# Optimization experiments

Measured on AMD Instinct MI355X. Metric: run time of the kernel, lower is better.

## Reference

```python
import jax, jax.numpy as jnp
import numpy as np

VOCAB, EMBED, SEQ, HID = 50000, 128, 200, 30
BATCH = 4096


def setup_inputs() -> dict:
    key = jax.random.key(0)
    ks = jax.random.split(key, 14)
    s = lambda fan_in: 1.0 / np.sqrt(fan_in)
    return {
        "tokens": jax.random.randint(ks[0], (BATCH, SEQ), 0, VOCAB, dtype=jnp.int32),
        "emb": jax.random.normal(ks[1], (VOCAB, EMBED), jnp.float32) * 0.05,
        "Wx": jax.random.normal(ks[2], (EMBED, HID), jnp.float32) * s(EMBED),
        "Wh": jax.random.normal(ks[3], (HID, HID), jnp.float32) * s(HID),
        "b_rnn": jnp.zeros((HID,), jnp.float32),
        "W1": jax.random.normal(ks[4], (HID, 128), jnp.float32) * s(HID),
        "b1": jnp.zeros((128,), jnp.float32),
        "W2": jax.random.normal(ks[5], (128, 64), jnp.float32) * s(128),
        "b2": jnp.zeros((64,), jnp.float32),
        "W3": jax.random.normal(ks[6], (64, 32), jnp.float32) * s(64),
        "b3": jnp.zeros((32,), jnp.float32),
        "Wo": jax.random.normal(ks[7], (32, 1), jnp.float32) * s(32),
        "bo": jnp.zeros((1,), jnp.float32),
    }


def reference(tokens, emb, Wx, Wh, b_rnn, W1, b1, W2, b2, W3, b3, Wo, bo):
    # Embedding lookup: [B, T, E]
    x = emb[tokens]
    # SimpleRNN (tanh), return last hidden state. Precompute input projection
    # once as a big GEMM, then scan the recurrence over time.
    xp = jnp.einsum("bte,eh->tbh", x, Wx) + b_rnn  # [T, B, H]
    h0 = jnp.zeros((tokens.shape[0], Wh.shape[0]), x.dtype)

    def step(h, xp_t):
        h_new = jnp.tanh(xp_t + h @ Wh)
        return h_new, None

    h_last, _ = jax.lax.scan(step, h0, xp)
    # Dense head (dropout layers are identity at inference).
    d1 = jax.nn.relu(h_last @ W1 + b1)
    d2 = jax.nn.relu(d1 @ W2 + b2)
    d3 = jax.nn.relu(d2 @ W3 + b3)
    return jax.nn.sigmoid(d3 @ Wo + bo)
```

## Files before the change

### kernel.cpp

```cpp
#include <hip/hip_runtime.h>
#include <math.h>

#define VOCAB 50000
#define EMBED 128
#define SEQ   200
#define HID   30
#define BATCH 4096

typedef float4 __attribute__((__may_alias__)) f4ma;
typedef unsigned int uint2v __attribute__((ext_vector_type(2)));

__device__ __forceinline__ float tanh_fast(float x) {
    float e = __expf(2.0f * x);
    return 1.0f - __fdividef(2.0f, e + 1.0f);
}
__device__ __forceinline__ float swz16_f(float x) {
    return __int_as_float(__builtin_amdgcn_ds_swizzle(__float_as_int(x), 0x401F));
}

__global__ __launch_bounds__(256, 2) void embproj_kernel(
    const float* __restrict__ emb, const float* __restrict__ Wx,
    const float* __restrict__ brnn, float* __restrict__ embP)
{
    int tid  = threadIdx.x;
    int wv   = tid >> 6;
    int l    = tid & 63;
    int j16  = l & 15;
    int p    = (l >> 4) & 1;
    int g    = l >> 5;
    int col  = j16 + 16 * g;
    int colc = (col < HID) ? col : (HID - 1);
    int k0   = 64 * p;

    float whx[64];
    #pragma unroll
    for (int i = 0; i < 64; ++i)
        whx[i] = Wx[(k0 + i) * HID + colc];
    float bj = brnn[colc];

    int base = (blockIdx.x * 4 + wv) * 25;

    float4 eA[16], eB[16];
    #define LOADROW(dst, v) { \
        int vc = min((v), VOCAB - 1); \
        const f4ma* e4 = (const f4ma*)(emb + (size_t)vc * EMBED + k0); \
        _Pragma("unroll") \
        for (int q = 0; q < 16; ++q) dst[q] = e4[q]; \
    }
    #define COMPUTE(src, v) { \
        float a0 = 0.f, a1 = 0.f, a2 = 0.f, a3 = 0.f; \
        _Pragma("unroll") \
        for (int q = 0; q < 16; ++q) { \
            a0 += src[q].x * whx[4*q+0]; \
            a1 += src[q].y * whx[4*q+1]; \
            a2 += src[q].z * whx[4*q+2]; \
            a3 += src[q].w * whx[4*q+3]; \
        } \
        float own  = (a0 + a1) + (a2 + a3); \
        float full = bj + (own + swz16_f(own)); \
        if (p == 0 && col < HID && (v) < VOCAB) \
            embP[(size_t)(v) * HID + col] = full; \
    }

    LOADROW(eA, base + 0);
    for (int r = 0; r < 25; r += 2) {
        LOADROW(eB, base + r + 1);
        COMPUTE(eA, base + r);
        LOADROW(eA, base + r + 2);
        COMPUTE(eB, base + r + 1);
    }
    #undef LOADROW
    #undef COMPUTE
}

__global__ __launch_bounds__(128) void rnn_head_kernel(
    const int* __restrict__ tokens, const float* __restrict__ embP,
    const float* __restrict__ Wh,
    const float* __restrict__ W1, const float* __restrict__ b1,
    const float* __restrict__ W2, const float* __restrict__ b2,
    const float* __restrict__ W3, const float* __restrict__ b3,
    const float* __restrict__ Wo, const float* __restrict__ bo,
    float* __restrict__ out)
{
    __shared__ __align__(16) float hL[4][32];
    __shared__ float d1L[4][128];
    __shared__ float d2L[4][64];

    int tid  = threadIdx.x;
    int wv   = tid >> 6;
    int l    = tid & 63;
    int j16  = l & 15;
    int row  = (l >> 4) & 1;
    int p    = l >> 5;
    int j    = j16 + 16 * p;
    int rloc = wv * 2 + row;
    int b    = blockIdx.x * 4 + rloc;

    const int* trow = tokens + (size_t)b * SEQ;
    int jc = (j < HID) ? j : (HID - 1);

    hL[rloc][j] = 0.0f;
    __builtin_amdgcn_sched_barrier(0);

    bool useR0;
    {
        unsigned li = (unsigned)l;
        uint2v rp = __builtin_amdgcn_permlane32_swap(li, li, false, false);
        useR0 = (rp[0] == (unsigned)(l ^ 32));
    }

    int cB = j16 + 16;
    float whA[16], whB[16];
    #pragma unroll
    for (int kk = 0; kk < 16; ++kk) {
        int k = 16 * p + kk;
        whA[kk] = (k < HID) ? Wh[k * HID + j16] : 0.0f;
        whB[kk] = (k < HID && cB < HID) ? Wh[k * HID + cB] : 0.0f;
    }

    float xq[8]; int tr[8];
    #pragma unroll
    for (int s = 0; s < 8; ++s) {
        xq[s] = embP[(size_t)trow[s] * HID + jc];
        tr[s] = trow[8 + s];
    }

    for (int t = 0; t < SEQ; t += 8) {
        #pragma unroll
        for (int s = 0; s < 8; ++s) {
            float hv[16];
            const f4ma* h4 = (const f4ma*)(&hL[rloc][16 * p]);
            #pragma unroll
            for (int qq = 0; qq < 4; ++qq) {
                f4ma hh = h4[qq];
                hv[4*qq+0] = hh.x; hv[4*qq+1] = hh.y;
                hv[4*qq+2] = hh.z; hv[4*qq+3] = hh.w;
            }
            float xp = xq[s];
            xq[s] = embP[(size_t)tr[s] * HID + jc];
            int tn = t + 16 + s; tn = (tn < SEQ) ? tn : SEQ - 1;
            tr[s] = trow[tn];

            float a0=0.f, a1=0.f, b0=0.f, b1=0.f;
            #pragma unroll
            for (int kk = 0; kk < 16; kk += 2) {
                a0 += hv[kk]   * whA[kk];
                a1 += hv[kk+1] * whA[kk+1];
                b0 += hv[kk]   * whB[kk];
                b1 += hv[kk+1] * whB[kk+1];
            }
            float pA = a0 + a1;
            float pB = b0 + b1;
            float own  = p ? pB : pA;
            float send = p ? pA : pB;
            unsigned si = __float_as_uint(send);
            uint2v sw = __builtin_amdgcn_permlane32_swap(si, si, false, false);
            float recv = __uint_as_float(useR0 ? sw[0] : sw[1]);
            float hn = tanh_fast(xp + (own + recv));
            if (j < HID) hL[rloc][j] = hn;
            __builtin_amdgcn_sched_barrier(0);
        }
    }

    {
        int half = l >> 5, j32 = l & 31;
        int rh = wv * 2 + half;
        int bB = blockIdx.x * 4 + rh;
        #pragma unroll
        for (int qq = 0; qq < 4; ++qq) {
            int c = j32 + 32 * qq;
            float acc = b1[c];
            #pragma unroll
            for (int k = 0; k < HID; ++k) acc += hL[rh][k] * W1[k * 128 + c];
            d1L[rh][c] = fmaxf(acc, 0.0f);
        }
        #pragma unroll
        for (int qq = 0; qq < 2; ++qq) {
            int c = j32 + 32 * qq;
            float acc = b2[c];
            #pragma unroll 8
            for (int k = 0; k < 128; ++k) acc += d1L[rh][k] * W2[k * 64 + c];
            d2L[rh][c] = fmaxf(acc, 0.0f);
        }
        float acc3 = b3[j32];
        #pragma unroll 8
        for (int k = 0; k < 64; ++k) acc3 += d2L[rh][k] * W3[k * 32 + j32];
        acc3 = fmaxf(acc3, 0.0f);
        float prod = acc3 * Wo[j32];
        #pragma unroll
        for (int m = 16; m > 0; m >>= 1) prod += __shfl_xor(prod, m, 32);
        if (j32 == 0) out[bB] = 1.0f / (1.0f + __expf(-(prod + bo[0])));
    }
}

extern "C" void kernel_launch(void* const* d_in, const int* in_sizes, int n_in,
                              void* d_out, int out_size, void* d_ws, size_t ws_size,
                              hipStream_t stream) {
    (void)in_sizes; (void)n_in; (void)out_size; (void)ws_size;
    const int*   tokens = (const int*)  d_in[0];
    const float* emb    = (const float*)d_in[1];
    const float* Wx     = (const float*)d_in[2];
    const float* Wh     = (const float*)d_in[3];
    const float* brnn   = (const float*)d_in[4];
    const float* W1     = (const float*)d_in[5];
    const float* b1     = (const float*)d_in[6];
    const float* W2     = (const float*)d_in[7];
    const float* b2     = (const float*)d_in[8];
    const float* W3     = (const float*)d_in[9];
    const float* b3     = (const float*)d_in[10];
    const float* Wo     = (const float*)d_in[11];
    const float* bo     = (const float*)d_in[12];
    float* out  = (float*)d_out;
    float* embP = (float*)d_ws;

    embproj_kernel<<<512, 256, 0, stream>>>(emb, Wx, brnn, embP);
    rnn_head_kernel<<<BATCH / 4, 128, 0, stream>>>(
        tokens, embP, Wh, W1, b1, W2, b2, W3, b3, Wo, bo, out);
}
```

Baseline: 95.74 us.

## Keep RNN hidden state in registers and broadcast via DPP row rotations

```diff
diff --git a/kernel.cpp b/kernel.cpp
--- a/kernel.cpp
+++ b/kernel.cpp
@@ -17,6 +17,7 @@
 __device__ __forceinline__ float swz16_f(float x) {
     return __int_as_float(__builtin_amdgcn_ds_swizzle(__float_as_int(x), 0x401F));
 }
+#define DPPI(x, ctrl) __builtin_amdgcn_update_dpp(0, (x), (ctrl), 0xF, 0xF, false)
 
 __global__ __launch_bounds__(256, 2) void embproj_kernel(
     const float* __restrict__ emb, const float* __restrict__ Wx,
@@ -82,7 +83,7 @@
     const float* __restrict__ Wo, const float* __restrict__ bo,
     float* __restrict__ out)
 {
-    __shared__ __align__(16) float hL[4][32];
+    __shared__ float hL[4][32];
     __shared__ float d1L[4][128];
     __shared__ float d2L[4][64];
 
@@ -99,9 +100,6 @@
     const int* trow = tokens + (size_t)b * SEQ;
     int jc = (j < HID) ? j : (HID - 1);
 
-    hL[rloc][j] = 0.0f;
-    __builtin_amdgcn_sched_barrier(0);
-
     bool useR0;
     {
         unsigned li = (unsigned)l;
@@ -109,13 +107,24 @@
         useR0 = (rp[0] == (unsigned)(l ^ 32));
     }
 
+    int kq[16];
+    kq[0]  = j16;
+    kq[1]  = DPPI(j16, 0x121);  kq[2]  = DPPI(j16, 0x122);
+    kq[3]  = DPPI(j16, 0x123);  kq[4]  = DPPI(j16, 0x124);
+    kq[5]  = DPPI(j16, 0x125);  kq[6]  = DPPI(j16, 0x126);
+    kq[7]  = DPPI(j16, 0x127);  kq[8]  = DPPI(j16, 0x128);
+    kq[9]  = DPPI(j16, 0x129);  kq[10] = DPPI(j16, 0x12A);
+    kq[11] = DPPI(j16, 0x12B);  kq[12] = DPPI(j16, 0x12C);
+    kq[13] = DPPI(j16, 0x12D);  kq[14] = DPPI(j16, 0x12E);
+    kq[15] = DPPI(j16, 0x12F);
+
     int cB = j16 + 16;
     float whA[16], whB[16];
     #pragma unroll
-    for (int kk = 0; kk < 16; ++kk) {
-        int k = 16 * p + kk;
-        whA[kk] = (k < HID) ? Wh[k * HID + j16] : 0.0f;
-        whB[kk] = (k < HID && cB < HID) ? Wh[k * HID + cB] : 0.0f;
+    for (int n = 0; n < 16; ++n) {
+        int k = 16 * p + kq[n];
+        whA[n] = (k < HID) ? Wh[k * HID + j16] : 0.0f;
+        whB[n] = (k < HID && cB < HID) ? Wh[k * HID + cB] : 0.0f;
     }
 
     float xq[8]; int tr[8];
@@ -125,17 +134,30 @@
         tr[s] = trow[8 + s];
     }
 
+    float hreg = 0.0f;
+
     for (int t = 0; t < SEQ; t += 8) {
         #pragma unroll
         for (int s = 0; s < 8; ++s) {
+            int hi = __float_as_int(hreg);
             float hv[16];
-            const f4ma* h4 = (const f4ma*)(&hL[rloc][16 * p]);
-            #pragma unroll
-            for (int qq = 0; qq < 4; ++qq) {
-                f4ma hh = h4[qq];
-                hv[4*qq+0] = hh.x; hv[4*qq+1] = hh.y;
-                hv[4*qq+2] = hh.z; hv[4*qq+3] = hh.w;
-            }
+            hv[0]  = hreg;
+            hv[1]  = __int_as_float(DPPI(hi, 0x121));
+            hv[2]  = __int_as_float(DPPI(hi, 0x122));
+            hv[3]  = __int_as_float(DPPI(hi, 0x123));
+            hv[4]  = __int_as_float(DPPI(hi, 0x124));
+            hv[5]  = __int_as_float(DPPI(hi, 0x125));
+            hv[6]  = __int_as_float(DPPI(hi, 0x126));
+            hv[7]  = __int_as_float(DPPI(hi, 0x127));
+            hv[8]  = __int_as_float(DPPI(hi, 0x128));
+            hv[9]  = __int_as_float(DPPI(hi, 0x129));
+            hv[10] = __int_as_float(DPPI(hi, 0x12A));
+            hv[11] = __int_as_float(DPPI(hi, 0x12B));
+            hv[12] = __int_as_float(DPPI(hi, 0x12C));
+            hv[13] = __int_as_float(DPPI(hi, 0x12D));
+            hv[14] = __int_as_float(DPPI(hi, 0x12E));
+            hv[15] = __int_as_float(DPPI(hi, 0x12F));
+
             float xp = xq[s];
             xq[s] = embP[(size_t)tr[s] * HID + jc];
             int tn = t + 16 + s; tn = (tn < SEQ) ? tn : SEQ - 1;
@@ -143,11 +165,11 @@
 
             float a0=0.f, a1=0.f, b0=0.f, b1=0.f;
             #pragma unroll
-            for (int kk = 0; kk < 16; kk += 2) {
-                a0 += hv[kk]   * whA[kk];
-                a1 += hv[kk+1] * whA[kk+1];
-                b0 += hv[kk]   * whB[kk];
-                b1 += hv[kk+1] * whB[kk+1];
+            for (int n = 0; n < 16; n += 2) {
+                a0 += hv[n]   * whA[n];
+                a1 += hv[n+1] * whA[n+1];
+                b0 += hv[n]   * whB[n];
+                b1 += hv[n+1] * whB[n+1];
             }
             float pA = a0 + a1;
             float pB = b0 + b1;
@@ -156,11 +178,12 @@
             unsigned si = __float_as_uint(send);
             uint2v sw = __builtin_amdgcn_permlane32_swap(si, si, false, false);
             float recv = __uint_as_float(useR0 ? sw[0] : sw[1]);
-            float hn = tanh_fast(xp + (own + recv));
-            if (j < HID) hL[rloc][j] = hn;
-            __builtin_amdgcn_sched_barrier(0);
+            hreg = tanh_fast(xp + (own + recv));
         }
     }
+
+    hL[rloc][j] = (j < HID) ? hreg : 0.0f;
+    __builtin_amdgcn_sched_barrier(0);
 
     {
         int half = l >> 5, j32 = l & 31;
```

After: 108.1 us. +12.9%, slower.
